# Optimization experiments

Measured on AMD Instinct MI355X. Metric: run time of the kernel, lower is better.

The kernel has to match this reference:

```python
import jax, jax.numpy as jnp
import numpy as np

B, T, D, H, DH = 2, 1024, 1024, 16, 64
DFF, V = 4096, 32000
L0, NLAT, WIN = 512, 4, 3
R, ALPHA = 8, 16
LATENT_ID = 31999


def _ln(x, s, b):
    m = x.mean(-1, keepdims=True)
    v = ((x - m) ** 2).mean(-1, keepdims=True)
    return (x - m) * jax.lax.rsqrt(v + 1e-5) * s + b


def _lm(embeds, Wpos, Wqkv, bqkv, Aq, Bq, Wo, bo, Ao, Bo, W1, b1, W2, b2,
        ln1_s, ln1_b, ln2_s, ln2_b, lnf_s, lnf_b):
    # single pre-LN transformer block with LoRA-merged c_attn/c_proj + final LN
    S = embeds.shape[1]
    sc = ALPHA / R
    h = embeds + Wpos[:S]
    a = _ln(h, ln1_s, ln1_b)
    qkv = a @ (Wqkv + sc * (Aq @ Bq)) + bqkv          # [B,S,3D]
    q, k, v = [t.reshape(B, S, H, DH) for t in jnp.split(qkv, 3, axis=-1)]
    scores = jnp.einsum('bqhd,bkhd->bhqk', q, k) / 8.0  # sqrt(DH)=8
    mask = jnp.tril(jnp.ones((S, S), bool))
    attn = jax.nn.softmax(jnp.where(mask, scores, -1e9), axis=-1)
    ctx = jnp.einsum('bhqk,bkhd->bqhd', attn, v).reshape(B, S, D)
    h = h + ctx @ (Wo + sc * (Ao @ Bo)) + bo
    m = _ln(h, ln2_s, ln2_b)
    h = h + jax.nn.gelu(m @ W1 + b1) @ W2 + b2
    return _ln(h, lnf_s, lnf_b)


def setup_inputs() -> dict:
    key = jax.random.key(0)
    ks = jax.random.split(key, 16)
    init = lambda k, shape, scale: jax.random.normal(k, shape, jnp.float32) * scale
    input_ids = jax.random.randint(ks[0], (B, T), 0, V)
    input_ids = input_ids.at[:, L0:L0 + NLAT].set(LATENT_ID)  # latent slots
    return {
        'input_ids': input_ids.astype(jnp.int32),
        'attention_mask': jnp.ones((B, T), jnp.int32),
        'labels': jax.random.randint(ks[1], (B, T), 0, V).astype(jnp.int32),
        'position_ids': jnp.broadcast_to(jnp.arange(T, dtype=jnp.int32), (B, T)),
        'embed': init(ks[2], (V, D), 0.02),
        'Wpos': init(ks[3], (T, D), 0.01),
        'Wqkv': init(ks[4], (D, 3 * D), 0.02), 'bqkv': jnp.zeros((3 * D,)),
        'Aq': init(ks[5], (D, R), 0.02), 'Bq': init(ks[6], (R, 3 * D), 0.02),
        'Wo': init(ks[7], (D, D), 0.02), 'bo': jnp.zeros((D,)),
        'Ao': init(ks[8], (D, R), 0.02), 'Bo': init(ks[9], (R, D), 0.02),
        'W1': init(ks[10], (D, DFF), 0.02), 'b1': jnp.zeros((DFF,)),
        'W2': init(ks[11], (DFF, D), 0.02), 'b2': jnp.zeros((D,)),
        'ln1_s': jnp.ones((D,)), 'ln1_b': jnp.zeros((D,)),
        'ln2_s': jnp.ones((D,)), 'ln2_b': jnp.zeros((D,)),
        'lnf_s': jnp.ones((D,)), 'lnf_b': jnp.zeros((D,)),
        'latent_w': jnp.zeros((WIN,)),
    }


def reference(input_ids, attention_mask, labels, position_ids, embed, Wpos,
              Wqkv, bqkv, Aq, Bq, Wo, bo, Ao, Bo, W1, b1, W2, b2,
              ln1_s, ln1_b, ln2_s, ln2_b, lnf_s, lnf_b, latent_w):
    lm = lambda e: _lm(e, Wpos, Wqkv, bqkv, Aq, Bq, Wo, bo, Ao, Bo,
                       W1, b1, W2, b2, ln1_s, ln1_b, ln2_s, ln2_b, lnf_s, lnf_b)
    embeds = embed[input_ids]                     # [B,T,D]
    parts = []
    for p in range(NLAT):                         # fixed small iterative-pass count
        start = 0 if p == 0 else L0 + p - 1       # segment processed this pass
        end = L0 + p
        hid = lm(embeds[:, :end])                 # frozen-prefix recompute == kv cache
        parts.append(hid[:, start:end] @ embed.T) # segment logits (tied lm_head)
        tok = L0 + p                              # latent slot filled this pass
        n = min(WIN, tok - start)                 # window clipped to segment offset
        w = jax.nn.softmax(latent_w[WIN - n:])    # softmax over last n weights
        vec = jnp.einsum('w,bwd->bd', w, hid[:, tok - n:tok])
        embeds = embeds.at[:, tok].set(vec)       # scatter into latent slot
    hid = lm(embeds)
    parts.append(hid[:, L0 + NLAT - 1:] @ embed.T)
    logits = jnp.concatenate(parts, axis=1)       # [B,T,V]
    logp = jax.nn.log_softmax(logits[:, :-1], axis=-1)
    nll = -jnp.take_along_axis(logp, labels[:, 1:, None].astype(jnp.int32), axis=-1)
    return nll.mean()
```

## Files before the change

### kernel.cpp

```cpp
#include <hip/hip_runtime.h>
#include <math.h>

#define B_   2
#define T_   1024
#define D_   1024
#define H_   16
#define DH_  64
#define DFF_ 4096
#define V_   32000
#define NTOK 2046
#define NCH  250

typedef __attribute__((ext_vector_type(8))) short short8;
typedef __attribute__((ext_vector_type(4))) float floatx4;

__device__ __forceinline__ unsigned short f2bf(float x) {
    unsigned int u = __float_as_uint(x);
    unsigned int r = (u + 0x7fffu + ((u >> 16) & 1u)) >> 16;
    return (unsigned short)r;
}

__device__ __forceinline__ float bf2f(unsigned short u) {
    return __uint_as_float((unsigned int)u << 16);
}

__device__ __forceinline__ void gld_lds16(void* lds, const void* g) {
    __builtin_amdgcn_global_load_lds(
        (const __attribute__((address_space(1))) void*)g,
        (__attribute__((address_space(3))) void*)lds, 16, 0, 0);
}

__device__ __forceinline__ float gelu_tanh(float x) {
    float x3 = x * x * x;
    return 0.5f * x * (1.0f + tanhf(0.7978845608028654f * (x + 0.044715f * x3)));
}

__global__ __launch_bounds__(256) void k_prep_w(const float* __restrict__ W,
        const float* __restrict__ A, const float* __restrict__ Bm,
        unsigned short* __restrict__ out, int K, int N, int lora) {
    __shared__ float t[64][65];
    int n0 = blockIdx.x * 64, k0 = blockIdx.y * 64;
    int tid = threadIdx.x;
    int nn = tid & 63, kb = tid >> 6;
    for (int i = 0; i < 16; i++) {
        int kk = kb * 16 + i;
        float v = W[(size_t)(k0 + kk) * N + n0 + nn];
        if (lora) {
            float s = 0.f;
#pragma unroll
            for (int r = 0; r < 8; r++) s += A[(k0 + kk) * 8 + r] * Bm[r * N + n0 + nn];
            v += 2.0f * s;
        }
        t[kk][nn] = v;
    }
    __syncthreads();
    int kk2 = tid & 63, nb = tid >> 6;
    for (int j = 0; j < 16; j++) {
        int nn2 = nb * 16 + j;
        out[(size_t)(n0 + nn2) * K + k0 + kk2] = f2bf(t[kk2][nn2]);
    }
}

__global__ void k_f2bf(const float* __restrict__ in, unsigned short* __restrict__ out, int n4) {
    int i = blockIdx.x * 256 + threadIdx.x;
    if (i >= n4) return;
    float4 v = ((const float4*)in)[i];
    ushort4 o;
    o.x = f2bf(v.x); o.y = f2bf(v.y); o.z = f2bf(v.z); o.w = f2bf(v.w);
    ((ushort4*)out)[i] = o;
}

__global__ void k_embed_gather(const int* __restrict__ ids, const float* __restrict__ embed,
                               float* __restrict__ embeds) {
    int bt = blockIdx.x;
    int d4 = threadIdx.x;
    int id = ids[bt];
    ((float4*)embeds)[(size_t)bt * 256 + d4] = ((const float4*)embed)[(size_t)id * 256 + d4];
}

__global__ __launch_bounds__(256) void k_ln(const float* __restrict__ in,
                                            const float* __restrict__ embeds, const float* __restrict__ Wpos,
                                            const float* __restrict__ sc, const float* __restrict__ bi,
                                            float* __restrict__ hout, float* __restrict__ outf,
                                            unsigned short* __restrict__ outbf,
                                            int c0, int range, int strided_bf) {
    int r = blockIdx.x;
    int b = r / range, pos = c0 + r % range;
    size_t rowoff = (size_t)(b * T_ + pos) * D_;
    int tid = threadIdx.x;
    float xv[4];
    if (embeds) {
#pragma unroll
        for (int j = 0; j < 4; j++) {
            int i = tid + j * 256;
            xv[j] = embeds[rowoff + i] + Wpos[(size_t)pos * D_ + i];
            hout[rowoff + i] = xv[j];
        }
    } else {
#pragma unroll
        for (int j = 0; j < 4; j++) xv[j] = in[rowoff + tid + j * 256];
    }
    float s1 = 0.f, s2 = 0.f;
#pragma unroll
    for (int j = 0; j < 4; j++) { s1 += xv[j]; s2 += xv[j] * xv[j]; }
    __shared__ float r1[256], r2[256];
    r1[tid] = s1; r2[tid] = s2; __syncthreads();
    for (int o = 128; o > 0; o >>= 1) {
        if (tid < o) { r1[tid] += r1[tid + o]; r2[tid] += r2[tid + o]; }
        __syncthreads();
    }
    float mean = r1[0] * (1.0f / D_);
    float var = r2[0] * (1.0f / D_) - mean * mean;
    float inv = rsqrtf(var + 1e-5f);
    size_t bfrow = strided_bf ? (size_t)(b * T_ + pos) : (size_t)r;
#pragma unroll
    for (int j = 0; j < 4; j++) {
        int i = tid + j * 256;
        float y = (xv[j] - mean) * inv * sc[i] + bi[i];
        if (outf) outf[rowoff + i] = y;
        outbf[bfrow * D_ + i] = f2bf(y);
    }
}

template <int MODE>
__global__ __launch_bounds__(256) void k_mgemm(const unsigned short* __restrict__ Abf,
        const unsigned short* __restrict__ Bt, const float* __restrict__ bias,
        float* __restrict__ o0, unsigned short* __restrict__ u0,
        unsigned short* __restrict__ u1, unsigned short* __restrict__ u2,
        int M, int N, int K, int c0, int range, int ksegs) {
    __shared__ short8 As0[256], Bs0[512];
    __shared__ short8 As1[256], Bs1[512];
    int tid = threadIdx.x;
    int lane = tid & 63, w = tid >> 6;
    int quad = lane >> 4, l15 = lane & 15;
    int row0 = blockIdx.y * 64, col0 = blockIdx.x * 128;
    int kseg = blockIdx.z;
    int Klen = K / ksegs;
    int ksoff = kseg * Klen;
    int wr = w >> 1, wc = w & 1;

    int arow = row0 + lane; if (arow >= M) arow = M - 1;
    const unsigned short* ga  = Abf + (size_t)arow * K + ksoff + w * 8;
    int bcol = col0 + (w & 1) * 64 + lane;
    const unsigned short* gb1 = Bt + (size_t)bcol * K + ksoff + (w >> 1) * 8;
    const unsigned short* gb2 = Bt + (size_t)bcol * K + ksoff + (2 + (w >> 1)) * 8;

    floatx4 acc[2][4];
#pragma unroll
    for (int i = 0; i < 2; i++)
#pragma unroll
        for (int j = 0; j < 4; j++)
#pragma unroll
            for (int k = 0; k < 4; k++) acc[i][j][k] = 0.f;

    int iters = Klen >> 5;

#define MSTAGE(AS, BS) \
    gld_lds16(&AS[w * 64],       ga); \
    gld_lds16(&BS[w * 64],       gb1); \
    gld_lds16(&BS[256 + w * 64], gb2); \
    ga += 32; gb1 += 32; gb2 += 32;

#define MCOMP(AS, BS) { \
    short8 af[2], bfv[4]; \
    _Pragma("unroll") \
    for (int mi = 0; mi < 2; mi++) af[mi] = AS[quad * 64 + wr * 32 + mi * 16 + l15]; \
    _Pragma("unroll") \
    for (int nj = 0; nj < 4; nj++) bfv[nj] = BS[quad * 128 + wc * 64 + nj * 16 + l15]; \
    _Pragma("unroll") \
    for (int mi = 0; mi < 2; mi++) \
        _Pragma("unroll") \
        for (int nj = 0; nj < 4; nj++) \
            acc[mi][nj] = __builtin_amdgcn_mfma_f32_16x16x32_bf16(af[mi], bfv[nj], acc[mi][nj], 0, 0, 0); }

#define MWVM3 \
    asm volatile("s_waitcnt vmcnt(3)" ::: "memory"); \
    __builtin_amdgcn_s_barrier(); \
    __builtin_amdgcn_sched_barrier(0);

#define MWLG \
    asm volatile("s_waitcnt lgkmcnt(0)" ::: "memory"); \
    __builtin_amdgcn_s_barrier(); \
    __builtin_amdgcn_sched_barrier(0);

    MSTAGE(As0, Bs0)
    for (int itp = 0; itp < (iters >> 1) - 1; ++itp) {
        MSTAGE(As1, Bs1) MWVM3 MCOMP(As0, Bs0) MWLG
        MSTAGE(As0, Bs0) MWVM3 MCOMP(As1, Bs1) MWLG
    }
    MSTAGE(As1, Bs1) MWVM3 MCOMP(As0, Bs0) MWLG
    asm volatile("s_waitcnt vmcnt(0)" ::: "memory");
    __builtin_amdgcn_s_barrier();
    __builtin_amdgcn_sched_barrier(0);
    MCOMP(As1, Bs1)

#undef MSTAGE
#undef MCOMP
#undef MWVM3
#undef MWLG

#pragma unroll
    for (int mi = 0; mi < 2; mi++)
#pragma unroll
        for (int reg = 0; reg < 4; reg++) {
            int r = row0 + wr * 32 + mi * 16 + quad * 4 + reg;
            if (r >= M) continue;
            int b = r / range, pos = c0 + r % range;
#pragma unroll
            for (int nj = 0; nj < 4; nj++) {
                int n = col0 + wc * 64 + nj * 16 + l15;
                if constexpr (MODE == 1) {
                    float v = acc[mi][nj][reg] + bias[n];
                    if (n < 1024) u0[(size_t)r * 1024 + n] = f2bf(v);
                    else if (n < 2048) u1[(size_t)(b * T_ + pos) * 1024 + (n - 1024)] = f2bf(v);
                    else u2[(size_t)(b * T_ + pos) * 1024 + (n - 2048)] = f2bf(v);
                } else if constexpr (MODE == 2) {
                    float v = acc[mi][nj][reg] + (kseg == 0 ? bias[n] : 0.f);
                    atomicAdd(&o0[(size_t)(b * T_ + pos) * D_ + n], v);
                } else if constexpr (MODE == 3) {
                    float v = acc[mi][nj][reg] + bias[n];
                    u0[(size_t)r * N + n] = f2bf(gelu_tanh(v));
                }
            }
        }
}

__global__ __launch_bounds__(256) void k_sp_part(const unsigned short* __restrict__ Abf,
        const unsigned short* __restrict__ Bt, float* __restrict__ pacc, int N, int K) {
    __shared__ unsigned short lds_a[2][256];
    __shared__ float lds_p[4][64][2];
    int tid = threadIdx.x, lane = tid & 63, w = tid >> 6;
    int n = blockIdx.x * 64 + lane;
    int kseg = blockIdx.y, k0 = kseg * 256;
    if (tid < 64) {
        int m = tid >> 5, j = tid & 31;
        *(short8*)&lds_a[m][j * 8] = *(const short8*)&Abf[(size_t)m * K + k0 + j * 8];
    }
    __syncthreads();
    int kw = w * 64;
    float a0 = 0.f, a1 = 0.f;
    const unsigned short* bp = Bt + (size_t)n * K + k0 + kw;
#pragma unroll
    for (int i = 0; i < 64; i += 8) {
        short8 bv  = *(const short8*)(bp + i);
        short8 av0 = *(const short8*)&lds_a[0][kw + i];
        short8 av1 = *(const short8*)&lds_a[1][kw + i];
#pragma unroll
        for (int j = 0; j < 8; j++) {
            float bf_ = bf2f((unsigned short)bv[j]);
            a0 += bf2f((unsigned short)av0[j]) * bf_;
            a1 += bf2f((unsigned short)av1[j]) * bf_;
        }
    }
    lds_p[w][lane][0] = a0;
    lds_p[w][lane][1] = a1;
    __syncthreads();
    if (tid < 128) {
        int l = tid & 63, m = tid >> 6;
        int nn = blockIdx.x * 64 + l;
        float acc = lds_p[0][l][m] + lds_p[1][l][m] + lds_p[2][l][m] + lds_p[3][l][m];
        pacc[((size_t)kseg * 2 + m) * N + nn] = acc;
    }
}

__global__ __launch_bounds__(256) void k_sp_add(const unsigned short* __restrict__ Abf,
        const unsigned short* __restrict__ Bt, const float* __restrict__ bias,
        float* __restrict__ o0, int N, int K, int c0) {
    __shared__ unsigned short lds_a[2][256];
    __shared__ float lds_p[4][64][2];
    int tid = threadIdx.x, lane = tid & 63, w = tid >> 6;
    int n = blockIdx.x * 64 + lane;
    int kseg = blockIdx.y, k0 = kseg * 256;
    if (tid < 64) {
        int m = tid >> 5, j = tid & 31;
        *(short8*)&lds_a[m][j * 8] = *(const short8*)&Abf[(size_t)m * K + k0 + j * 8];
    }
    __syncthreads();
    int kw = w * 64;
    float a0 = 0.f, a1 = 0.f;
    const unsigned short* bp = Bt + (size_t)n * K + k0 + kw;
#pragma unroll
    for (int i = 0; i < 64; i += 8) {
        short8 bv  = *(const short8*)(bp + i);
        short8 av0 = *(const short8*)&lds_a[0][kw + i];
        short8 av1 = *(const short8*)&lds_a[1][kw + i];
#pragma unroll
        for (int j = 0; j < 8; j++) {
            float bf_ = bf2f((unsigned short)bv[j]);
            a0 += bf2f((unsigned short)av0[j]) * bf_;
            a1 += bf2f((unsigned short)av1[j]) * bf_;
        }
    }
    lds_p[w][lane][0] = a0;
    lds_p[w][lane][1] = a1;
    __syncthreads();
    if (tid < 128) {
        int l = tid & 63, m = tid >> 6;
        int nn = blockIdx.x * 64 + l;
        float acc = lds_p[0][l][m] + lds_p[1][l][m] + lds_p[2][l][m] + lds_p[3][l][m];
        if (kseg == 0) acc += bias[nn];
        atomicAdd(&o0[(size_t)(m * T_ + c0) * D_ + nn], acc);
    }
}

template <int MODE>
__global__ void k_sp_fin(const float* __restrict__ pacc, const float* __restrict__ bias,
        unsigned short* __restrict__ u0, unsigned short* __restrict__ u1,
        unsigned short* __restrict__ u2, int N, int nseg, int c0) {
    int idx = blockIdx.x * 256 + threadIdx.x;
    if (idx >= 2 * N) return;
    int m = idx / N, n = idx % N;
    float s = 0.f;
    for (int k = 0; k < nseg; k++) s += pacc[((size_t)k * 2 + m) * N + n];
    s += bias[n];
    if constexpr (MODE == 4) {
        if (n < 1024) u0[(size_t)m * 1024 + n] = f2bf(s);
        else if (n < 2048) u1[(size_t)(m * T_ + c0) * 1024 + (n - 1024)] = f2bf(s);
        else {
            int id2 = n - 2048, h = id2 >> 6, d = id2 & 63;
            u2[(size_t)((m * 16 + h) * 64 + d) * T_ + c0] = f2bf(s);
        }
    } else {
        u0[(size_t)m * N + n] = f2bf(gelu_tanh(s));
    }
}

__global__ __launch_bounds__(256) void k_vtrans(const unsigned short* __restrict__ vcbf,
        unsigned short* __restrict__ vtc, int c0, int range) {
    __shared__ unsigned short ts[64][72];
    int pt = blockIdx.x, h = blockIdx.y, b = blockIdx.z;
    int t = threadIdx.x;
#pragma unroll
    for (int i = 0; i < 2; i++) {
        int idx = t + i * 256;
        int p = idx >> 3, c8 = idx & 7;
        int pos = c0 + pt * 64 + p;
        if (pos < c0 + range) {
            short8 v = *(const short8*)&vcbf[(size_t)(b * T_ + pos) * D_ + h * 64 + c8 * 8];
            *(short8*)&ts[p][c8 * 8] = v;
        }
    }
    __syncthreads();
#pragma unroll
    for (int i = 0; i < 2; i++) {
        int idx = t + i * 256;
        int d = idx >> 3, p8 = idx & 7;
        unsigned short tmp[8];
#pragma unroll
        for (int j = 0; j < 8; j++) tmp[j] = ts[p8 * 8 + j][d];
        int pos0 = c0 + pt * 64 + p8 * 8;
        size_t rb = (size_t)((b * 16 + h) * 64 + d) * T_;
        if (pos0 + 7 < c0 + range) {
            *(short8*)&vtc[rb + pos0] = *(short8*)tmp;
        } else {
            for (int j = 0; j < 8; j++)
                if (pos0 + j < c0 + range) vtc[rb + pos0 + j] = tmp[j];
        }
    }
}

__global__ __launch_bounds__(256) void k_fattn(const unsigned short* __restrict__ qbf,
        const unsigned short* __restrict__ kcbf, const unsigned short* __restrict__ vtc,
        unsigned short* __restrict__ ctxbf, int c0, int range) {
    __shared__ unsigned short pw[4][16][72];
    int tid = threadIdx.x;
    int w = tid >> 6, lane = tid & 63, quad = lane >> 4, l15 = lane & 15;
    int qt = blockIdx.x, h = blockIdx.y, b = blockIdx.z;
    int q0 = qt * 64 + w * 16;
    if (q0 >= range) return;
    int qtop = q0 + 15; if (qtop >= range) qtop = range - 1;
    int nkt = (c0 + qtop) / 64 + 1;

    int qrow = q0 + l15; if (qrow >= range) qrow = range - 1;
    const unsigned short* qp = qbf + (size_t)(b * range + qrow) * D_ + h * 64 + quad * 8;
    short8 aq0 = *(const short8*)qp;
    short8 aq1 = *(const short8*)(qp + 32);

    floatx4 oacc[4];
#pragma unroll
    for (int dg = 0; dg < 4; dg++)
#pragma unroll
        for (int r = 0; r < 4; r++) oacc[dg][r] = 0.f;
    float m_r[4] = {-1e30f, -1e30f, -1e30f, -1e30f};
    float l_r[4] = {0.f, 0.f, 0.f, 0.f};

    const unsigned short* kb_p = kcbf + (size_t)b * T_ * D_ + h * 64 + quad * 8;
    const unsigned short* vb_p = vtc + (size_t)((b * 16 + h) * 64 + l15) * T_ + quad * 8;

    for (int kt = 0; kt < nkt; kt++) {
        int kb = kt * 64;
        floatx4 s[4];
#pragma unroll
        for (int g = 0; g < 4; g++) {
            const unsigned short* kp = kb_p + (size_t)(kb + g * 16 + l15) * D_;
            short8 bk0 = *(const short8*)kp;
            short8 bk1 = *(const short8*)(kp + 32);
            floatx4 z; z[0] = 0.f; z[1] = 0.f; z[2] = 0.f; z[3] = 0.f;
            z = __builtin_amdgcn_mfma_f32_16x16x32_bf16(aq0, bk0, z, 0, 0, 0);
            s[g] = __builtin_amdgcn_mfma_f32_16x16x32_bf16(aq1, bk1, z, 0, 0, 0);
        }
#pragma unroll
        for (int r = 0; r < 4; r++) {
            int qpos = c0 + q0 + quad * 4 + r;
            float mx = -1e30f;
#pragma unroll
            for (int g = 0; g < 4; g++) {
                int kpos = kb + g * 16 + l15;
                float sv = (kpos <= qpos) ? s[g][r] * 0.125f : -1e30f;
                s[g][r] = sv; mx = fmaxf(mx, sv);
            }
            mx = fmaxf(mx, __shfl_xor(mx, 1));
            mx = fmaxf(mx, __shfl_xor(mx, 2));
            mx = fmaxf(mx, __shfl_xor(mx, 4));
            mx = fmaxf(mx, __shfl_xor(mx, 8));
            float mn = fmaxf(m_r[r], mx);
            float alpha = __expf(m_r[r] - mn);
            m_r[r] = mn;
            float ls = 0.f;
#pragma unroll
            for (int g = 0; g < 4; g++) {
                float p = __expf(s[g][r] - mn);
                s[g][r] = p; ls += p;
            }
            ls += __shfl_xor(ls, 1);
            ls += __shfl_xor(ls, 2);
            ls += __shfl_xor(ls, 4);
            ls += __shfl_xor(ls, 8);
            l_r[r] = l_r[r] * alpha + ls;
#pragma unroll
            for (int dg = 0; dg < 4; dg++) oacc[dg][r] *= alpha;
        }
#pragma unroll
        for (int g = 0; g < 4; g++)
#pragma unroll
            for (int r = 0; r < 4; r++)
                pw[w][quad * 4 + r][g * 16 + l15] = f2bf(s[g][r]);
        short8 ap0 = *(const short8*)&pw[w][l15][quad * 8];
        short8 ap1 = *(const short8*)&pw[w][l15][32 + quad * 8];
#pragma unroll
        for (int dg = 0; dg < 4; dg++) {
            const unsigned short* vp = vb_p + (size_t)(dg * 16) * T_ + kb;
            short8 bv0 = *(const short8*)vp;
            short8 bv1 = *(const short8*)(vp + 32);
            oacc[dg] = __builtin_amdgcn_mfma_f32_16x16x32_bf16(ap0, bv0, oacc[dg], 0, 0, 0);
            oacc[dg] = __builtin_amdgcn_mfma_f32_16x16x32_bf16(ap1, bv1, oacc[dg], 0, 0, 0);
        }
    }
#pragma unroll
    for (int dg = 0; dg < 4; dg++)
#pragma unroll
        for (int r = 0; r < 4; r++) {
            int qloc = q0 + quad * 4 + r;
            if (qloc < range)
                ctxbf[(size_t)(b * range + qloc) * D_ + h * 64 + dg * 16 + l15] =
                    f2bf(oacc[dg][r] / l_r[r]);
        }
}

__global__ void k_latent0(const float* __restrict__ hid, const float* __restrict__ lw,
                          float* __restrict__ embeds) {
    int idx = blockIdx.x * 256 + threadIdx.x;
    if (idx >= B_ * D_) return;
    int b = idx / D_, d = idx % D_;
    float w0 = lw[0], w1 = lw[1], w2 = lw[2];
    float mx = fmaxf(w0, fmaxf(w1, w2));
    float e0 = __expf(w0 - mx), e1 = __expf(w1 - mx), e2 = __expf(w2 - mx);
    float inv = 1.0f / (e0 + e1 + e2);
    float v = (e0 * hid[(size_t)(b * T_ + 509) * D_ + d] +
               e1 * hid[(size_t)(b * T_ + 510) * D_ + d] +
               e2 * hid[(size_t)(b * T_ + 511) * D_ + d]) * inv;
    embeds[(size_t)(b * T_ + 512) * D_ + d] = v;
}

__global__ void k_latent1(const float* __restrict__ hid, float* __restrict__ embeds, int tok) {
    int idx = blockIdx.x * 256 + threadIdx.x;
    if (idx >= B_ * D_) return;
    int b = idx / D_, d = idx % D_;
    embeds[(size_t)(b * T_ + tok) * D_ + d] = hid[(size_t)(b * T_ + tok - 1) * D_ + d];
}

__global__ __launch_bounds__(256) void k_loss1m(const unsigned short* __restrict__ hidbf,
        const unsigned short* __restrict__ embedbf, const int* __restrict__ labels,
        float* __restrict__ partm, float* __restrict__ parts, float* __restrict__ llogit) {
    __shared__ short8 As0[512], Bs0[512];
    __shared__ short8 As1[512], Bs1[512];
    __shared__ int lds_lab[128];
    __shared__ float lds_pm[128][2];
    __shared__ float lds_ps[128][2];
    int tid = threadIdx.x;
    int lane = tid & 63, w = tid >> 6;
    int quad = lane >> 4, l15 = lane & 15;
    int chunk = blockIdx.y;
    int row0 = blockIdx.x * 128, v0 = chunk * 128;
    int rh = (w >> 1) * 64, ch = (w & 1) * 64;

    if (tid < 128) {
        int tok = row0 + tid;
        lds_lab[tid] = (tok < NTOK) ? labels[tok + 1 + (tok >= 1023)] : -1;
    }

    int cA0 = w * 128 + lane, cA1 = cA0 + 64;
    int rA0 = cA0 & 127, kgA0 = cA0 >> 7;
    int rA1 = cA1 & 127, kgA1 = cA1 >> 7;
    int tokA0 = row0 + rA0; if (tokA0 >= NTOK) tokA0 = NTOK - 1;
    int tokA1 = row0 + rA1; if (tokA1 >= NTOK) tokA1 = NTOK - 1;
    const unsigned short* ga0 = hidbf + (size_t)(tokA0 + (tokA0 >= 1023)) * D_ + kgA0 * 8;
    const unsigned short* ga1 = hidbf + (size_t)(tokA1 + (tokA1 >= 1023)) * D_ + kgA1 * 8;
    const unsigned short* gb0 = embedbf + (size_t)(v0 + rA0) * D_ + kgA0 * 8;
    const unsigned short* gb1 = embedbf + (size_t)(v0 + rA1) * D_ + kgA1 * 8;

    floatx4 acc[4][4];
#pragma unroll
    for (int i = 0; i < 4; i++)
#pragma unroll
        for (int j = 0; j < 4; j++)
#pragma unroll
            for (int k = 0; k < 4; k++) acc[i][j][k] = 0.f;

#define LSTAGE(AS, BS) \
    gld_lds16(&AS[w * 128],      ga0); \
    gld_lds16(&AS[w * 128 + 64], ga1); \
    gld_lds16(&BS[w * 128],      gb0); \
    gld_lds16(&BS[w * 128 + 64], gb1); \
    ga0 += 32; ga1 += 32; gb0 += 32; gb1 += 32;

#define LCOMP(AS, BS) { \
    short8 af[4], bfv[4]; \
    _Pragma("unroll") \
    for (int mi = 0; mi < 4; mi++) af[mi] = AS[quad * 128 + rh + mi * 16 + l15]; \
    _Pragma("unroll") \
    for (int nj = 0; nj < 4; nj++) bfv[nj] = BS[quad * 128 + ch + nj * 16 + l15]; \
    _Pragma("unroll") \
    for (int mi = 0; mi < 4; mi++) \
        _Pragma("unroll") \
        for (int nj = 0; nj < 4; nj++) \
            acc[mi][nj] = __builtin_amdgcn_mfma_f32_16x16x32_bf16(af[mi], bfv[nj], acc[mi][nj], 0, 0, 0); }

#define WAIT_VM4_BAR \
    asm volatile("s_waitcnt vmcnt(4)" ::: "memory"); \
    __builtin_amdgcn_s_barrier(); \
    __builtin_amdgcn_sched_barrier(0);

#define WAIT_LGKM_BAR \
    asm volatile("s_waitcnt lgkmcnt(0)" ::: "memory"); \
    __builtin_amdgcn_s_barrier(); \
    __builtin_amdgcn_sched_barrier(0);

    LSTAGE(As0, Bs0)
    for (int itp = 0; itp < 15; ++itp) {
        LSTAGE(As1, Bs1)
        WAIT_VM4_BAR
        LCOMP(As0, Bs0)
        WAIT_LGKM_BAR
        LSTAGE(As0, Bs0)
        WAIT_VM4_BAR
        LCOMP(As1, Bs1)
        WAIT_LGKM_BAR
    }
    LSTAGE(As1, Bs1)
    WAIT_VM4_BAR
    LCOMP(As0, Bs0)
    WAIT_LGKM_BAR
    asm volatile("s_waitcnt vmcnt(0)" ::: "memory");
    __builtin_amdgcn_s_barrier();
    __builtin_amdgcn_sched_barrier(0);
    LCOMP(As1, Bs1)

#undef LSTAGE
#undef LCOMP
#undef WAIT_VM4_BAR
#undef WAIT_LGKM_BAR

#pragma unroll
    for (int mi = 0; mi < 4; mi++)
#pragma unroll
        for (int reg = 0; reg < 4; reg++) {
            int rloc = rh + mi * 16 + quad * 4 + reg;
            int lab = lds_lab[rloc];
            float vm = -1e30f;
#pragma unroll
            for (int nj = 0; nj < 4; nj++) {
                float v = acc[mi][nj][reg];
                int vcol = v0 + ch + nj * 16 + l15;
                if (vcol == lab) llogit[row0 + rloc] = v;
                vm = fmaxf(vm, v);
            }
            for (int off = 1; off < 16; off <<= 1) vm = fmaxf(vm, __shfl_xor(vm, off));
            float ss = 0.f;
#pragma unroll
            for (int nj = 0; nj < 4; nj++) ss += __expf(acc[mi][nj][reg] - vm);
            for (int off = 1; off < 16; off <<= 1) ss += __shfl_xor(ss, off);
            if (l15 == 0) { lds_pm[rloc][ch >> 6] = vm; lds_ps[rloc][ch >> 6] = ss; }
        }
    __syncthreads();
    if (tid < 128) {
        int tok = row0 + tid;
        if (tok < NTOK) {
            float m0 = lds_pm[tid][0], m1 = lds_pm[tid][1];
            float M = fmaxf(m0, m1);
            float S = lds_ps[tid][0] * __expf(m0 - M) + lds_ps[tid][1] * __expf(m1 - M);
            partm[(size_t)chunk * NTOK + tok] = M;
            parts[(size_t)chunk * NTOK + tok] = S;
        }
    }
}

__global__ void k_loss2a(const float* __restrict__ partm, const float* __restrict__ parts,
                         const float* __restrict__ ll, float* __restrict__ nll) {
    int tok = blockIdx.x * 256 + threadIdx.x;
    if (tok >= NTOK) return;
    float M = -1e30f;
    for (int c = 0; c < NCH; c++) M = fmaxf(M, partm[(size_t)c * NTOK + tok]);
    float S = 0.f;
    for (int c = 0; c < NCH; c++)
        S += parts[(size_t)c * NTOK + tok] * __expf(partm[(size_t)c * NTOK + tok] - M);
    nll[tok] = logf(S) + M - ll[tok];
}

__global__ __launch_bounds__(256) void k_loss2b(const float* __restrict__ nll, float* __restrict__ out) {
    __shared__ float red[256];
    int tid = threadIdx.x;
    float s = 0.f;
    for (int i = tid; i < NTOK; i += 256) s += nll[i];
    red[tid] = s; __syncthreads();
    for (int o = 128; o > 0; o >>= 1) {
        if (tid < o) red[tid] += red[tid + o];
        __syncthreads();
    }
    if (tid == 0) out[0] = red[0] / (float)NTOK;
}

extern "C" void kernel_launch(void* const* d_in, const int* in_sizes, int n_in,
                              void* d_out, int out_size, void* d_ws, size_t ws_size,
                              hipStream_t stream) {
    const int*   input_ids = (const int*)d_in[0];
    const int*   labels    = (const int*)d_in[2];
    const float* embed     = (const float*)d_in[4];
    const float* Wpos      = (const float*)d_in[5];
    const float* Wqkv      = (const float*)d_in[6];
    const float* bqkv      = (const float*)d_in[7];
    const float* Aq        = (const float*)d_in[8];
    const float* Bq        = (const float*)d_in[9];
    const float* Wo        = (const float*)d_in[10];
    const float* bo        = (const float*)d_in[11];
    const float* Ao        = (const float*)d_in[12];
    const float* Bo        = (const float*)d_in[13];
    const float* W1        = (const float*)d_in[14];
    const float* b1        = (const float*)d_in[15];
    const float* W2        = (const float*)d_in[16];
    const float* b2        = (const float*)d_in[17];
    const float* ln1_s     = (const float*)d_in[18];
    const float* ln1_b     = (const float*)d_in[19];
    const float* ln2_s     = (const float*)d_in[20];
    const float* ln2_b     = (const float*)d_in[21];
    const float* lnf_s     = (const float*)d_in[22];
    const float* lnf_b     = (const float*)d_in[23];
    const float* latent_w  = (const float*)d_in[24];

    char* base = (char*)d_ws;
    size_t off = 0;
    auto alloc = [&](size_t bytes) { void* p = base + off; off += (bytes + 255) & ~255ULL; return p; };

    float* embeds  = (float*)alloc((size_t)B_ * T_ * D_ * 4);
    float* hbuf    = (float*)alloc((size_t)B_ * T_ * D_ * 4);
    float* hidbuf  = (float*)alloc((size_t)B_ * T_ * D_ * 4);
    float* partm   = (float*)alloc((size_t)NCH * NTOK * 4);
    float* parts_  = (float*)alloc((size_t)NCH * NTOK * 4);
    float* llogit  = (float*)alloc((size_t)NTOK * 4);
    float* nllbuf  = (float*)alloc((size_t)NTOK * 4);
    float* pacc    = (float*)alloc((size_t)16 * 2 * 4096 * 4);
    unsigned short* wqkvT  = (unsigned short*)alloc((size_t)3072 * 1024 * 2);
    unsigned short* woT    = (unsigned short*)alloc((size_t)1024 * 1024 * 2);
    unsigned short* W1T    = (unsigned short*)alloc((size_t)4096 * 1024 * 2);
    unsigned short* W2T    = (unsigned short*)alloc((size_t)1024 * 4096 * 2);
    unsigned short* embedbf = (unsigned short*)alloc((size_t)V_ * D_ * 2);
    unsigned short* hidbf  = (unsigned short*)alloc((size_t)B_ * T_ * D_ * 2);
    unsigned short* abf    = (unsigned short*)alloc((size_t)1024 * D_ * 2);
    unsigned short* ctxbf  = (unsigned short*)alloc((size_t)1024 * D_ * 2);
    unsigned short* ffbw   = (unsigned short*)alloc((size_t)1024 * DFF_ * 2);
    unsigned short* qbf    = (unsigned short*)alloc((size_t)1024 * D_ * 2);
    unsigned short* kcbf   = (unsigned short*)alloc((size_t)B_ * T_ * D_ * 2);
    unsigned short* vcbf   = (unsigned short*)alloc((size_t)B_ * T_ * D_ * 2);
    unsigned short* vtc    = (unsigned short*)alloc((size_t)B_ * H_ * DH_ * T_ * 2);

    k_prep_w<<<dim3(3072 / 64, 1024 / 64), 256, 0, stream>>>(Wqkv, Aq, Bq, wqkvT, 1024, 3072, 1);
    k_prep_w<<<dim3(1024 / 64, 1024 / 64), 256, 0, stream>>>(Wo, Ao, Bo, woT, 1024, 1024, 1);
    k_prep_w<<<dim3(4096 / 64, 1024 / 64), 256, 0, stream>>>(W1, nullptr, nullptr, W1T, 1024, 4096, 0);
    k_prep_w<<<dim3(1024 / 64, 4096 / 64), 256, 0, stream>>>(W2, nullptr, nullptr, W2T, 4096, 1024, 0);
    k_f2bf<<<(V_ * D_ / 4 + 255) / 256, 256, 0, stream>>>(embed, embedbf, V_ * D_ / 4);
    k_embed_gather<<<B_ * T_, 256, 0, stream>>>(input_ids, embed, embeds);

    auto run_pass = [&](int c0, int c1) {
        int range = c1 - c0;
        int Mr = B_ * range;
        int gy = (Mr + 63) / 64;
        int qt = (range + 63) / 64;
        k_ln<<<Mr, 256, 0, stream>>>(nullptr, embeds, Wpos, ln1_s, ln1_b, hbuf, nullptr, abf, c0, range, 0);
        if (range == 1) {
            k_sp_part<<<dim3(48, 4), 256, 0, stream>>>(abf, wqkvT, pacc, 3072, 1024);
            k_sp_fin<4><<<24, 256, 0, stream>>>(pacc, bqkv, qbf, kcbf, vtc, 3072, 4, c0);
            k_fattn<<<dim3(1, H_, B_), 256, 0, stream>>>(qbf, kcbf, vtc, ctxbf, c0, 1);
            k_sp_add<<<dim3(16, 4), 256, 0, stream>>>(ctxbf, woT, bo, hbuf, 1024, 1024, c0);
            k_ln<<<Mr, 256, 0, stream>>>(hbuf, nullptr, nullptr, ln2_s, ln2_b, nullptr, nullptr, abf, c0, range, 0);
            k_sp_part<<<dim3(64, 4), 256, 0, stream>>>(abf, W1T, pacc, 4096, 1024);
            k_sp_fin<3><<<32, 256, 0, stream>>>(pacc, b1, ffbw, nullptr, nullptr, 4096, 4, c0);
            k_sp_add<<<dim3(16, 16), 256, 0, stream>>>(ffbw, W2T, b2, hbuf, 1024, 4096, c0);
        } else {
            k_mgemm<1><<<dim3(3072 / 128, gy), 256, 0, stream>>>(abf, wqkvT, bqkv, nullptr, qbf, kcbf, vcbf,
                                                                 Mr, 3072, 1024, c0, range, 1);
            k_vtrans<<<dim3(qt, H_, B_), 256, 0, stream>>>(vcbf, vtc, c0, range);
            k_fattn<<<dim3(qt, H_, B_), 256, 0, stream>>>(qbf, kcbf, vtc, ctxbf, c0, range);
            k_mgemm<2><<<dim3(1024 / 128, gy, 4), 256, 0, stream>>>(ctxbf, woT, bo, hbuf, nullptr, nullptr, nullptr,
                                                                    Mr, 1024, 1024, c0, range, 4);
            k_ln<<<Mr, 256, 0, stream>>>(hbuf, nullptr, nullptr, ln2_s, ln2_b, nullptr, nullptr, abf, c0, range, 0);
            k_mgemm<3><<<dim3(4096 / 128, gy), 256, 0, stream>>>(abf, W1T, b1, nullptr, ffbw, nullptr, nullptr,
                                                                 Mr, 4096, 1024, c0, range, 1);
            k_mgemm<2><<<dim3(1024 / 128, gy, 4), 256, 0, stream>>>(ffbw, W2T, b2, hbuf, nullptr, nullptr, nullptr,
                                                                    Mr, 1024, 4096, c0, range, 4);
        }
        k_ln<<<Mr, 256, 0, stream>>>(hbuf, nullptr, nullptr, lnf_s, lnf_b, nullptr, hidbuf, hidbf, c0, range, 1);
    };

    run_pass(0, 512);
    k_latent0<<<(B_ * D_ + 255) / 256, 256, 0, stream>>>(hidbuf, latent_w, embeds);
    run_pass(512, 513);
    k_latent1<<<(B_ * D_ + 255) / 256, 256, 0, stream>>>(hidbuf, embeds, 513);
    run_pass(513, 514);
    k_latent1<<<(B_ * D_ + 255) / 256, 256, 0, stream>>>(hidbuf, embeds, 514);
    run_pass(514, 515);
    k_latent1<<<(B_ * D_ + 255) / 256, 256, 0, stream>>>(hidbuf, embeds, 515);
    run_pass(515, 1024);

    k_loss1m<<<dim3((NTOK + 127) / 128, NCH), 256, 0, stream>>>(hidbf, embedbf, labels, partm, parts_, llogit);
    k_loss2a<<<(NTOK + 255) / 256, 256, 0, stream>>>(partm, parts_, llogit, nllbuf);
    k_loss2b<<<1, 256, 0, stream>>>(nllbuf, (float*)d_out);
}
```

Measured before the change: 1.173 ms.

## Enlarge loss GEMM tiles to 256x256 with 512 threads and swizzled block order

The fused logits/log-sum-exp kernel moves from 128x128 tiles with 4 waves to 256x256 tiles with 8 waves, each wave computing 128x64. This halves the number of vocab chunks and raises operand reuse per LDS load. Block indices are also remapped so that consecutive blocks share a vocab chunk across row tiles, which should improve L2 reuse of the embedding matrix. In exchange the kernel needs more LDS and registers per block (8x4 accumulators), which lowers occupancy.

```diff
diff --git a/kernel.cpp b/kernel.cpp
--- a/kernel.cpp
+++ b/kernel.cpp
@@ -9,7 +9,7 @@
 #define DFF_ 4096
 #define V_   32000
 #define NTOK 2046
-#define NCH  250
+#define NCH  125
 
 typedef __attribute__((ext_vector_type(8))) short short8;
 typedef __attribute__((ext_vector_type(4))) float floatx4;
@@ -479,59 +479,63 @@
     embeds[(size_t)(b * T_ + tok) * D_ + d] = hid[(size_t)(b * T_ + tok - 1) * D_ + d];
 }
 
-__global__ __launch_bounds__(256) void k_loss1m(const unsigned short* __restrict__ hidbf,
+__global__ __launch_bounds__(512, 2) void k_loss1m(const unsigned short* __restrict__ hidbf,
         const unsigned short* __restrict__ embedbf, const int* __restrict__ labels,
         float* __restrict__ partm, float* __restrict__ parts, float* __restrict__ llogit) {
-    __shared__ short8 As0[512], Bs0[512];
-    __shared__ short8 As1[512], Bs1[512];
-    __shared__ int lds_lab[128];
-    __shared__ float lds_pm[128][2];
-    __shared__ float lds_ps[128][2];
+    __shared__ short8 As0[1024], Bs0[1024];
+    __shared__ short8 As1[1024], Bs1[1024];
+    __shared__ int lds_lab[256];
+    __shared__ float lds_pm[256][4];
+    __shared__ float lds_ps[256][4];
     int tid = threadIdx.x;
     int lane = tid & 63, w = tid >> 6;
     int quad = lane >> 4, l15 = lane & 15;
-    int chunk = blockIdx.y;
-    int row0 = blockIdx.x * 128, v0 = chunk * 128;
-    int rh = (w >> 1) * 64, ch = (w & 1) * 64;
-
-    if (tid < 128) {
+    int flat = blockIdx.y * 8 + blockIdx.x;
+    int swz = (flat & 7) * 125 + (flat >> 3);
+    int chunk = swz >> 3;
+    int rtile = swz & 7;
+    int row0 = rtile * 256, v0 = chunk * 256;
+    int wr = w >> 2, wc = w & 3;
+
+    if (tid < 256) {
         int tok = row0 + tid;
         lds_lab[tid] = (tok < NTOK) ? labels[tok + 1 + (tok >= 1023)] : -1;
     }
 
-    int cA0 = w * 128 + lane, cA1 = cA0 + 64;
-    int rA0 = cA0 & 127, kgA0 = cA0 >> 7;
-    int rA1 = cA1 & 127, kgA1 = cA1 >> 7;
-    int tokA0 = row0 + rA0; if (tokA0 >= NTOK) tokA0 = NTOK - 1;
-    int tokA1 = row0 + rA1; if (tokA1 >= NTOK) tokA1 = NTOK - 1;
-    const unsigned short* ga0 = hidbf + (size_t)(tokA0 + (tokA0 >= 1023)) * D_ + kgA0 * 8;
-    const unsigned short* ga1 = hidbf + (size_t)(tokA1 + (tokA1 >= 1023)) * D_ + kgA1 * 8;
-    const unsigned short* gb0 = embedbf + (size_t)(v0 + rA0) * D_ + kgA0 * 8;
-    const unsigned short* gb1 = embedbf + (size_t)(v0 + rA1) * D_ + kgA1 * 8;
-
-    floatx4 acc[4][4];
-#pragma unroll
-    for (int i = 0; i < 4; i++)
+    const unsigned short* ga[2];
+    const unsigned short* gb[2];
+#pragma unroll
+    for (int j = 0; j < 2; j++) {
+        int c = (w * 2 + j) * 64 + lane;
+        int rowi = c & 255, kg = c >> 8;
+        int tokA = row0 + rowi; if (tokA >= NTOK) tokA = NTOK - 1;
+        ga[j] = hidbf + (size_t)(tokA + (tokA >= 1023)) * D_ + kg * 8;
+        gb[j] = embedbf + (size_t)(v0 + rowi) * D_ + kg * 8;
+    }
+
+    floatx4 acc[8][4];
+#pragma unroll
+    for (int i = 0; i < 8; i++)
 #pragma unroll
         for (int j = 0; j < 4; j++)
 #pragma unroll
             for (int k = 0; k < 4; k++) acc[i][j][k] = 0.f;
 
 #define LSTAGE(AS, BS) \
-    gld_lds16(&AS[w * 128],      ga0); \
-    gld_lds16(&AS[w * 128 + 64], ga1); \
-    gld_lds16(&BS[w * 128],      gb0); \
-    gld_lds16(&BS[w * 128 + 64], gb1); \
-    ga0 += 32; ga1 += 32; gb0 += 32; gb1 += 32;
+    gld_lds16(&AS[(w * 2 + 0) * 64], ga[0]); \
+    gld_lds16(&AS[(w * 2 + 1) * 64], ga[1]); \
+    gld_lds16(&BS[(w * 2 + 0) * 64], gb[0]); \
+    gld_lds16(&BS[(w * 2 + 1) * 64], gb[1]); \
+    ga[0] += 32; ga[1] += 32; gb[0] += 32; gb[1] += 32;
 
 #define LCOMP(AS, BS) { \
-    short8 af[4], bfv[4]; \
+    short8 af[8], bfv[4]; \
     _Pragma("unroll") \
-    for (int mi = 0; mi < 4; mi++) af[mi] = AS[quad * 128 + rh + mi * 16 + l15]; \
+    for (int mi = 0; mi < 8; mi++) af[mi] = AS[quad * 256 + wr * 128 + mi * 16 + l15]; \
     _Pragma("unroll") \
-    for (int nj = 0; nj < 4; nj++) bfv[nj] = BS[quad * 128 + ch + nj * 16 + l15]; \
+    for (int nj = 0; nj < 4; nj++) bfv[nj] = BS[quad * 256 + wc * 64 + nj * 16 + l15]; \
     _Pragma("unroll") \
-    for (int mi = 0; mi < 4; mi++) \
+    for (int mi = 0; mi < 8; mi++) \
         _Pragma("unroll") \
         for (int nj = 0; nj < 4; nj++) \
             acc[mi][nj] = __builtin_amdgcn_mfma_f32_16x16x32_bf16(af[mi], bfv[nj], acc[mi][nj], 0, 0, 0); }
@@ -572,16 +576,16 @@
 #undef WAIT_LGKM_BAR
 
 #pragma unroll
-    for (int mi = 0; mi < 4; mi++)
+    for (int mi = 0; mi < 8; mi++)
 #pragma unroll
         for (int reg = 0; reg < 4; reg++) {
-            int rloc = rh + mi * 16 + quad * 4 + reg;
+            int rloc = wr * 128 + mi * 16 + quad * 4 + reg;
             int lab = lds_lab[rloc];
             float vm = -1e30f;
 #pragma unroll
             for (int nj = 0; nj < 4; nj++) {
                 float v = acc[mi][nj][reg];
-                int vcol = v0 + ch + nj * 16 + l15;
+                int vcol = v0 + wc * 64 + nj * 16 + l15;
                 if (vcol == lab) llogit[row0 + rloc] = v;
                 vm = fmaxf(vm, v);
             }
@@ -590,15 +594,19 @@
 #pragma unroll
             for (int nj = 0; nj < 4; nj++) ss += __expf(acc[mi][nj][reg] - vm);
             for (int off = 1; off < 16; off <<= 1) ss += __shfl_xor(ss, off);
-            if (l15 == 0) { lds_pm[rloc][ch >> 6] = vm; lds_ps[rloc][ch >> 6] = ss; }
+            if (l15 == 0) { lds_pm[rloc][wc] = vm; lds_ps[rloc][wc] = ss; }
         }
     __syncthreads();
-    if (tid < 128) {
+    if (tid < 256) {
         int tok = row0 + tid;
         if (tok < NTOK) {
-            float m0 = lds_pm[tid][0], m1 = lds_pm[tid][1];
+            float m0 = fmaxf(lds_pm[tid][0], lds_pm[tid][1]);
+            float m1 = fmaxf(lds_pm[tid][2], lds_pm[tid][3]);
             float M = fmaxf(m0, m1);
-            float S = lds_ps[tid][0] * __expf(m0 - M) + lds_ps[tid][1] * __expf(m1 - M);
+            float S = lds_ps[tid][0] * __expf(lds_pm[tid][0] - M)
+                    + lds_ps[tid][1] * __expf(lds_pm[tid][1] - M)
+                    + lds_ps[tid][2] * __expf(lds_pm[tid][2] - M)
+                    + lds_ps[tid][3] * __expf(lds_pm[tid][3] - M);
             partm[(size_t)chunk * NTOK + tok] = M;
             parts[(size_t)chunk * NTOK + tok] = S;
         }
@@ -731,7 +739,7 @@
     k_latent1<<<(B_ * D_ + 255) / 256, 256, 0, stream>>>(hidbuf, embeds, 515);
     run_pass(515, 1024);
 
-    k_loss1m<<<dim3((NTOK + 127) / 128, NCH), 256, 0, stream>>>(hidbf, embedbf, labels, partm, parts_, llogit);
+    k_loss1m<<<dim3(8, NCH), 512, 0, stream>>>(hidbf, embedbf, labels, partm, parts_, llogit);
     k_loss2a<<<(NTOK + 255) / 256, 256, 0, stream>>>(partm, parts_, llogit, nllbuf);
     k_loss2b<<<1, 256, 0, stream>>>(nllbuf, (float*)d_out);
 }
```

New measurement: 1.130 ms. 1.04x faster.
